# Performance work log

Measured on AMD Instinct MI355X. Metric: run time of the kernel, lower is better.

## Reference

```python
import jax, jax.numpy as jnp
import numpy as np

NUM_EXPERTS = 16
TOP_K = 2
FFT_LEN = 512
SEQ_LEN = 512
PRED_LEN = 720
MOE_TEMP = 1.0


def setup_inputs() -> dict:
    key = jax.random.key(0)
    ks = jax.random.split(key, 5)
    x = jax.random.normal(ks[0], (8192, SEQ_LEN), dtype=jnp.float32)
    # gating network: Linear(fft_len//2 -> num_experts)
    gw = jax.random.normal(ks[1], (NUM_EXPERTS, FFT_LEN // 2), dtype=jnp.float32) * (1.0 / np.sqrt(FFT_LEN // 2))
    gb = jnp.zeros((NUM_EXPERTS,), dtype=jnp.float32)
    # experts: RLinear = instance-norm (RevIN) + Linear(seq->pred), stacked
    ew = jax.random.normal(ks[2], (NUM_EXPERTS, SEQ_LEN, PRED_LEN), dtype=jnp.float32) * (1.0 / np.sqrt(SEQ_LEN))
    eb = jnp.zeros((NUM_EXPERTS, PRED_LEN), dtype=jnp.float32)
    return {"x": x, "gw": gw, "gb": gb, "ew": ew, "eb": eb}


def periodogram(x, n):
    # x: [B, L] -> normalized power spectrum [B, n//2]
    x0 = x - jnp.mean(x, axis=1, keepdims=True)
    dft = jnp.fft.fft(x0, n=n, axis=1) / jnp.sqrt(jnp.asarray(n, x.dtype))
    I = jnp.abs(dft[:, : n // 2]) ** 2
    s = jnp.sum(I, axis=1, keepdims=True)
    s = jnp.where(s == 0, 1.0, s)
    return I / s


def expert_apply(x, ew, eb):
    # RLinear: instance normalize, linear map, de-normalize
    mu = jnp.mean(x, axis=1, keepdims=True)
    sd = jnp.std(x, axis=1, keepdims=True) + 1e-5
    xn = (x - mu) / sd  # [B, L]
    # all experts densely: [B,L] x [E,L,P] -> [E,B,P]
    y = jnp.einsum('bl,elp->ebp', xn, ew) + eb[:, None, :]
    return y * sd[None] + mu[None]  # [E, B, P]


def reference(x, gw, gb, ew, eb):
    I = periodogram(x, FFT_LEN)  # [B, n//2]
    gate = (I @ gw.T + gb) / MOE_TEMP  # eval mode: divide by temp, no noise
    topk_vals, topk_idx = jax.lax.top_k(gate, TOP_K)  # [B, k]
    gates = jax.nn.softmax(topk_vals, axis=1)  # [B, k]
    expert_out = expert_apply(x, ew, eb)  # [E, B, P]
    # gather selected experts: [B, k, P]
    sel = jnp.take_along_axis(
        jnp.transpose(expert_out, (1, 0, 2)), topk_idx[:, :, None], axis=1
    )
    return jnp.sum(gates[:, :, None] * sel, axis=1)  # [B, P]
```

## Files before the change

### kernel.cpp

```cpp
#include <hip/hip_runtime.h>
#include <hip/hip_bf16.h>
#include <math.h>

#define NEXP  16
#define SEQ   512
#define PRED  720
#define NROWS 8192
#define NFREQ 256

typedef __bf16 bf16x8 __attribute__((ext_vector_type(8)));
typedef float  f32x16 __attribute__((ext_vector_type(16)));

__device__ __forceinline__ void gload_lds16(const void* g, void* l) {
    __builtin_amdgcn_global_load_lds(
        (const __attribute__((address_space(1))) unsigned int*)g,
        (__attribute__((address_space(3))) unsigned int*)l, 16, 0, 0);
}

__global__ __launch_bounds__(256) void k_transpose_ew(const float* __restrict__ ew,
                                                      __hip_bfloat16* __restrict__ ewt)
{
    __shared__ float tile[32][33];
    const int e  = blockIdx.z;
    const int p0 = blockIdx.x * 32;
    const int l0 = blockIdx.y * 32;
    const int tx = threadIdx.x & 31;
    const int ty = threadIdx.x >> 5;
    const float* src = ew + (size_t)e * SEQ * PRED;
#pragma unroll
    for (int i = 0; i < 4; ++i) {
        int l = l0 + ty + i * 8;
        int p = p0 + tx;
        tile[ty + i * 8][tx] = (p < PRED) ? src[(size_t)l * PRED + p] : 0.f;
    }
    __syncthreads();
    __hip_bfloat16* dst = ewt + (size_t)e * PRED * SEQ;
#pragma unroll
    for (int i = 0; i < 4; ++i) {
        int p = p0 + ty + i * 8;
        int l = l0 + tx;
        if (p < PRED) dst[(size_t)p * SEQ + l] = __float2bfloat16(tile[tx][ty + i * 8]);
    }
}

__global__ __launch_bounds__(256) void k_build_dft(__hip_bfloat16* __restrict__ bthi,
                                                   __hip_bfloat16* __restrict__ btlo)
{
    const int tid  = blockIdx.x * 256 + threadIdx.x;
    const int f    = tid >> 9;
    const int lidx = tid & 511;
    const int m    = (f * lidx) & 511;

    constexpr double Cj[9] = {0.9999247018391445033, 0.9996988186962042201,
                              0.9987954562051723927, 0.9951847266721968862,
                              0.9807852804032304491, 0.9238795325112867561,
                              0.7071067811865475244, 0.0, -1.0};
    constexpr double Sj[9] = {0.0122715382857199261, 0.0245412285229122880,
                              0.0490676743274180143, 0.0980171403295606020,
                              0.1950903220161282678, 0.3826834323650897717,
                              0.7071067811865475244, 1.0, 0.0};
    double cr = 1.0, ci = 0.0;
#pragma unroll
    for (int j = 0; j < 9; ++j) {
        const bool on = (m >> j) & 1;
        const double mr = on ? Cj[j] : 1.0;
        const double mi = on ? Sj[j] : 0.0;
        const double nr = cr * mr - ci * mi;
        ci = cr * mi + ci * mr;
        cr = nr;
    }

    const size_t c0 = (size_t)(2 * f) * 512 + lidx;
    const size_t c1 = (size_t)(2 * f + 1) * 512 + lidx;
    {
        __hip_bfloat16 h = __float2bfloat16((float)cr);
        float hif = __bfloat162float(h);
        bthi[c0] = h;
        btlo[c0] = __float2bfloat16((float)(cr - (double)hif));
    }
    {
        __hip_bfloat16 h = __float2bfloat16((float)ci);
        float hif = __bfloat162float(h);
        bthi[c1] = h;
        btlo[c1] = __float2bfloat16((float)(ci - (double)hif));
    }
}

__global__ __launch_bounds__(256) void k_stats(const float* __restrict__ x,
                                               __hip_bfloat16* __restrict__ xn,
                                               __hip_bfloat16* __restrict__ xnlo,
                                               float* __restrict__ meta)
{
    const int t  = threadIdx.x;
    const int wv = t >> 6, l = t & 63;
    const int b  = blockIdx.x * 4 + wv;
    const float* xr = x + (size_t)b * SEQ;

    const float4 v0 = *(const float4*)(xr + l * 8);
    const float4 v1 = *(const float4*)(xr + l * 8 + 4);
    const double d0 = v0.x, d1 = v0.y, d2 = v0.z, d3 = v0.w;
    const double d4 = v1.x, d5 = v1.y, d6 = v1.z, d7 = v1.w;

    double s1 = ((d0 + d1) + (d2 + d3)) + ((d4 + d5) + (d6 + d7));
    double s2 = ((d0 * d0 + d1 * d1) + (d2 * d2 + d3 * d3)) +
                ((d4 * d4 + d5 * d5) + (d6 * d6 + d7 * d7));
#pragma unroll
    for (int off = 1; off < 64; off <<= 1) {
        s1 += __shfl_xor(s1, off);
        s2 += __shfl_xor(s2, off);
    }
    const double mu = s1 * (1.0 / 512.0);
    double var = s2 * (1.0 / 512.0) - mu * mu;
    if (var < 0.0) var = 0.0;
    const double sd = sqrt(var) + 1e-5, inv = 1.0 / sd;

    unsigned int hw[4], lw[4];
#define CONV(j, dj)                                                         \
    {                                                                       \
        double xnd = (dj - mu) * inv;                                       \
        __hip_bfloat16 h = __float2bfloat16((float)xnd);                    \
        float hif = __bfloat162float(h);                                    \
        __hip_bfloat16 lo = __float2bfloat16((float)(xnd - (double)hif));   \
        unsigned int hb = *(unsigned short*)&h;                             \
        unsigned int lb = *(unsigned short*)&lo;                            \
        if ((j & 1) == 0) { hw[j >> 1] = hb; lw[j >> 1] = lb; }             \
        else { hw[j >> 1] |= hb << 16; lw[j >> 1] |= lb << 16; }            \
    }
    CONV(0, d0) CONV(1, d1) CONV(2, d2) CONV(3, d3)
    CONV(4, d4) CONV(5, d5) CONV(6, d6) CONV(7, d7)
#undef CONV
    *(uint4*)(xn   + (size_t)b * SEQ + l * 8) = uint4{hw[0], hw[1], hw[2], hw[3]};
    *(uint4*)(xnlo + (size_t)b * SEQ + l * 8) = uint4{lw[0], lw[1], lw[2], lw[3]};

    if (l == 0) {
        meta[b * 4 + 0] = (float)mu;
        meta[b * 4 + 3] = (float)sd;
    }
}

__global__ __launch_bounds__(256, 2) void k_dft_gemm(
    const __hip_bfloat16* __restrict__ xn, const __hip_bfloat16* __restrict__ xnlo,
    const __hip_bfloat16* __restrict__ bthi, const __hip_bfloat16* __restrict__ btlo,
    float* __restrict__ Iout)
{
    const int rt = blockIdx.y;
    const int ct = blockIdx.x;

    __shared__ __align__(16) __hip_bfloat16 As[2][128][64];
    __shared__ __align__(16) __hip_bfloat16 Bs[2][128][64];

    const int t  = threadIdx.x;
    const int wv = t >> 6, l = t & 63;
    const int srow = l >> 3, schk = l & 7;

    size_t aoff[4], boff[4];
#pragma unroll
    for (int i = 0; i < 4; ++i) {
        const int r   = wv * 32 + i * 8 + srow;
        const int swz = (r & 7) ^ ((r & 8) >> 1);
        aoff[i] = (size_t)(rt * 128 + r) * SEQ + (size_t)(schk ^ swz) * 8;
        boff[i] = (size_t)(ct * 128 + r) * SEQ + (size_t)(schk ^ swz) * 8;
    }

#define DSTAGE(buf, kk) do {                                                   \
    const int pass_ = (kk) >> 3;                                               \
    const int koff_ = ((kk) & 7) * 64;                                         \
    const __hip_bfloat16* ap_ = (pass_ == 1) ? xnlo : xn;                      \
    const __hip_bfloat16* bp_ = (pass_ == 2) ? btlo : bthi;                    \
    _Pragma("unroll")                                                          \
    for (int i_ = 0; i_ < 4; ++i_)                                             \
        gload_lds16(ap_ + aoff[i_] + koff_, &As[buf][wv * 32 + i_ * 8][0]);    \
    _Pragma("unroll")                                                          \
    for (int i_ = 0; i_ < 4; ++i_)                                             \
        gload_lds16(bp_ + boff[i_] + koff_, &Bs[buf][wv * 32 + i_ * 8][0]);    \
} while (0)

    f32x16 acc[2][2];
#pragma unroll
    for (int mi = 0; mi < 2; ++mi)
#pragma unroll
        for (int ni = 0; ni < 2; ++ni)
#pragma unroll
            for (int q = 0; q < 16; ++q) acc[mi][ni][q] = 0.f;

    const int wrow = (wv >> 1) * 64, wcol = (wv & 1) * 64;
    const int fl = l & 31, fh = l >> 5;
    const int rswz = (fl & 7) ^ ((fl & 8) >> 1);

    DSTAGE(0, 0);
    __syncthreads();
    int cur = 0;
    for (int kt = 0; kt < 24; ++kt) {
        if (kt < 23) DSTAGE(cur ^ 1, kt + 1);
#pragma unroll
        for (int ks = 0; ks < 4; ++ks) {
            const int g  = ks * 2 + fh;
            const int cc = (g ^ rswz) * 8;
            const bf16x8 a0 = *(const bf16x8*)&As[cur][wrow + fl][cc];
            const bf16x8 a1 = *(const bf16x8*)&As[cur][wrow + 32 + fl][cc];
            const bf16x8 b0 = *(const bf16x8*)&Bs[cur][wcol + fl][cc];
            const bf16x8 b1 = *(const bf16x8*)&Bs[cur][wcol + 32 + fl][cc];
            acc[0][0] = __builtin_amdgcn_mfma_f32_32x32x16_bf16(a0, b0, acc[0][0], 0, 0, 0);
            acc[0][1] = __builtin_amdgcn_mfma_f32_32x32x16_bf16(a0, b1, acc[0][1], 0, 0, 0);
            acc[1][0] = __builtin_amdgcn_mfma_f32_32x32x16_bf16(a1, b0, acc[1][0], 0, 0, 0);
            acc[1][1] = __builtin_amdgcn_mfma_f32_32x32x16_bf16(a1, b1, acc[1][1], 0, 0, 0);
        }
        __syncthreads();
        cur ^= 1;
    }
#undef DSTAGE

    const int crow_base = 4 * fh;
#pragma unroll
    for (int ni = 0; ni < 2; ++ni) {
        const int col = ct * 128 + wcol + ni * 32 + fl;
#pragma unroll
        for (int mi = 0; mi < 2; ++mi) {
#pragma unroll
            for (int q = 0; q < 16; ++q) {
                const float v = acc[mi][ni][q];
                const float w = __shfl_xor(v, 1);
                if ((fl & 1) == 0) {
                    const int rl = wrow + mi * 32 + (q & 3) + 8 * (q >> 2) + crow_base;
                    Iout[(size_t)(rt * 128 + rl) * NFREQ + (col >> 1)] = v * v + w * w;
                }
            }
        }
    }
}

__global__ __launch_bounds__(256) void k_gatefin(const float* __restrict__ Iout,
                                                 const float* __restrict__ gw,
                                                 const float* __restrict__ gb,
                                                 float* __restrict__ meta,
                                                 int* __restrict__ eidx,
                                                 int* __restrict__ redo,
                                                 int* __restrict__ nredo)
{
    __shared__ float gws[NEXP * 257];
    __shared__ float Pw[4][256];
    __shared__ float Gs[4][16];

    const int t  = threadIdx.x;
    const int wv = t >> 6, l = t & 63;
    const int b  = blockIdx.x * 4 + wv;

    for (int i = t; i < NEXP * NFREQ; i += 256)
        gws[(i >> 8) * 257 + (i & 255)] = gw[i];
    __syncthreads();

    const float* Ir = Iout + (size_t)b * NFREQ;
    const float i0 = Ir[l], i1 = Ir[64 + l], i2 = Ir[128 + l], i3 = Ir[192 + l];
    Pw[wv][l] = i0; Pw[wv][64 + l] = i1; Pw[wv][128 + l] = i2; Pw[wv][192 + l] = i3;
    float ps = (i0 + i1) + (i2 + i3);
#pragma unroll
    for (int off = 1; off < 64; off <<= 1) ps += __shfl_xor(ps, off);

    const int e = l >> 2, kb = l & 3;
    float acc = 0.f;
#pragma unroll 8
    for (int j = 0; j < 64; ++j) {
        const int k = kb + 4 * j;
        acc += Pw[wv][k] * gws[e * 257 + k];
    }
    acc += __shfl_xor(acc, 1);
    acc += __shfl_xor(acc, 2);
    if (kb == 0) Gs[wv][e] = acc;

    if (l == 0) {
        const float sdiv  = (ps == 0.f) ? 1.f : ps;
        const float inv_s = 1.f / sdiv;
        float b1 = -1e30f, b2 = -1e30f, b3 = -1e30f;
        int i1b = 0, i2b = 0;
#pragma unroll
        for (int i = 0; i < NEXP; ++i) {
            float v = Gs[wv][i] * inv_s + gb[i];
            if (v > b1)      { b3 = b2; b2 = b1; i2b = i1b; b1 = v; i1b = i; }
            else if (v > b2) { b3 = b2; b2 = v; i2b = i; }
            else if (v > b3) { b3 = v; }
        }
        if (b2 - b3 < 1e-4f * fmaxf(1.f, fabsf(b1))) {
            const int r = atomicAdd(nredo, 1);
            redo[r] = b;
        } else {
            const float sd = meta[b * 4 + 3];
            const float ee = __expf(b2 - b1);
            const float w0 = 1.f / (1.f + ee);
            const float w1 = ee / (1.f + ee);
            meta[b * 4 + 1] = w0 * sd;
            meta[b * 4 + 2] = w1 * sd;
            eidx[b * 2 + 0] = i1b;
            eidx[b * 2 + 1] = i2b;
        }
    }
}

__global__ __launch_bounds__(256, 4) void k_gate64(const float* __restrict__ x,
                                                   const float* __restrict__ gw,
                                                   const float* __restrict__ gb,
                                                   float* __restrict__ meta,
                                                   int* __restrict__ eidx,
                                                   const int* __restrict__ redo,
                                                   const int* __restrict__ nredo)
{
    __shared__ double Pw[4][256];
    __shared__ double Gs[4][16];

    const int t  = threadIdx.x;
    const int wv = t >> 6, l = t & 63;
    const int n  = *nredo;

    for (int it = blockIdx.x * 4 + wv; it < n; it += gridDim.x * 4) {
        const int b = redo[it];
        const float* xr = x + (size_t)b * SEQ;

        double s1 = 0.0, s2 = 0.0;
#define DLOADV(n_) double vr##n_ = (double)xr[64 * n_ + l]; s1 += vr##n_; s2 += vr##n_ * vr##n_;
        DLOADV(0) DLOADV(1) DLOADV(2) DLOADV(3) DLOADV(4) DLOADV(5) DLOADV(6) DLOADV(7)
#undef DLOADV
        double vi0, vi1, vi2, vi3, vi4, vi5, vi6, vi7;

#pragma unroll
        for (int off = 1; off < 64; off <<= 1) {
            s1 += __shfl_xor(s1, off);
            s2 += __shfl_xor(s2, off);
        }
        const double mu = s1 * (1.0 / 512.0);
        double var = s2 * (1.0 / 512.0) - mu * mu;
        if (var < 0.0) var = 0.0;
        const double sd = sqrt(var) + 1e-5;

#define DSUB(n_) vr##n_ -= mu;
        DSUB(0) DSUB(1) DSUB(2) DSUB(3) DSUB(4) DSUB(5) DSUB(6) DSUB(7)
#undef DSUB

        {
            const double C = 0.70710678118654752440084436210485;
            double a0 = vr0 + vr4, a1 = vr1 + vr5, a2 = vr2 + vr6, a3 = vr3 + vr7;
            double d0 = vr0 - vr4, d1 = vr1 - vr5, d2 = vr2 - vr6, d3 = vr3 - vr7;
            double c0 = a0 + a2, c2 = a0 - a2, c1 = a1 + a3;
            double c3i = a3 - a1;
            double e1r = C * (d1 - d3), e1i = -C * (d1 + d3);
            vr0 = c0 + c1;   vi0 = 0.0;
            vr1 = c0 - c1;   vi1 = 0.0;
            vr2 = c2;        vi2 = c3i;
            vr3 = c2;        vi3 = -c3i;
            vr4 = d0 + e1r;  vi4 = -d2 + e1i;
            vr5 = d0 - e1r;  vi5 = -d2 - e1i;
            vr6 = d0 - e1r;  vi6 =  d2 + e1i;
            vr7 = d0 + e1r;  vi7 =  d2 - e1i;
        }

        double w1r = 1.0, w1i = 0.0;
        {
            constexpr double Cr[6] = {0.9999247018391445033, 0.9996988186962042201,
                                      0.9987954562051723927, 0.9951847266721968862,
                                      0.9807852804032304491, 0.9238795325112867561};
            constexpr double Ci[6] = {-0.0122715382857199261, -0.0245412285229122880,
                                      -0.0490676743274180143, -0.0980171403295606020,
                                      -0.1950903220161282678, -0.3826834323650897717};
#pragma unroll
            for (int j = 0; j < 6; ++j) {
                const bool on = (l >> j) & 1;
                const double mr = on ? Cr[j] : 1.0;
                const double mi = on ? Ci[j] : 0.0;
                const double nr = w1r * mr - w1i * mi;
                w1i = w1r * mi + w1i * mr;
                w1r = nr;
            }
        }

        {
            double wkr = w1r, wki = w1i;
#define DTWID(n_) { double tr_ = vr##n_ * wkr - vi##n_ * wki; \
                    vi##n_ = vr##n_ * wki + vi##n_ * wkr; vr##n_ = tr_; }
#define DWSTEP() { double nr_ = wkr * w1r - wki * w1i; \
                   wki = wkr * w1i + wki * w1r; wkr = nr_; }
            DTWID(4) DWSTEP() DTWID(2) DWSTEP() DTWID(6) DWSTEP() DTWID(1)
            DWSTEP() DTWID(5) DWSTEP() DTWID(3) DWSTEP() DTWID(7)
#undef DTWID
#undef DWSTEP
        }

        double twr, twi;
        {
            double w2r = w1r * w1r - w1i * w1i, w2i = 2.0 * w1r * w1i;
            double w4r = w2r * w2r - w2i * w2i, w4i = 2.0 * w2r * w2i;
            twr = w4r * w4r - w4i * w4i; twi = 2.0 * w4r * w4i;
        }
#define DBF(R, I, h, hi, ter, tei) { \
        double br_ = __shfl_xor(R, h); double bi_ = __shfl_xor(I, h); \
        double dr_ = hi ? (R - br_) : (R + br_); \
        double di_ = hi ? (I - bi_) : (I + bi_); \
        R = dr_ * ter - di_ * tei; I = dr_ * tei + di_ * ter; }
#define DSTAGE(hc) { \
        const bool hi_ = (l & hc) != 0; \
        const double ter_ = hi_ ? twr : 1.0; \
        const double tei_ = hi_ ? twi : 0.0; \
        DBF(vr0, vi0, hc, hi_, ter_, tei_) DBF(vr1, vi1, hc, hi_, ter_, tei_) \
        DBF(vr2, vi2, hc, hi_, ter_, tei_) DBF(vr3, vi3, hc, hi_, ter_, tei_) \
        DBF(vr4, vi4, hc, hi_, ter_, tei_) DBF(vr5, vi5, hc, hi_, ter_, tei_) \
        DBF(vr6, vi6, hc, hi_, ter_, tei_) DBF(vr7, vi7, hc, hi_, ter_, tei_) \
        double ntr_ = twr * twr - twi * twi; twi = 2.0 * twr * twi; twr = ntr_; }
        DSTAGE(32) DSTAGE(16) DSTAGE(8) DSTAGE(4) DSTAGE(2) DSTAGE(1)
#undef DSTAGE
#undef DBF

        const int k2 = (int)(__brev((unsigned)l) >> 26);
        double ps = 0.0;
        if ((l & 1) == 0) {
            const int kb = 8 * k2;
            double P;
            P = vr0 * vr0 + vi0 * vi0; ps += P; Pw[wv][0 + kb] = P;
            P = vr1 * vr1 + vi1 * vi1; ps += P; Pw[wv][4 + kb] = P;
            P = vr2 * vr2 + vi2 * vi2; ps += P; Pw[wv][2 + kb] = P;
            P = vr3 * vr3 + vi3 * vi3; ps += P; Pw[wv][6 + kb] = P;
            P = vr4 * vr4 + vi4 * vi4; ps += P; Pw[wv][1 + kb] = P;
            P = vr5 * vr5 + vi5 * vi5; ps += P; Pw[wv][5 + kb] = P;
            P = vr6 * vr6 + vi6 * vi6; ps += P; Pw[wv][3 + kb] = P;
            P = vr7 * vr7 + vi7 * vi7; ps += P; Pw[wv][7 + kb] = P;
        }
#pragma unroll
        for (int off = 1; off < 64; off <<= 1) ps += __shfl_xor(ps, off);

        {
            const int e = l >> 2, kb = l & 3;
            double acc = 0.0;
#pragma unroll 8
            for (int j = 0; j < 64; ++j) {
                int k = kb + 4 * j;
                acc += Pw[wv][k] * (double)gw[e * NFREQ + k];
            }
            acc += __shfl_xor(acc, 1);
            acc += __shfl_xor(acc, 2);
            if (kb == 0) Gs[wv][e] = acc;
        }

        if (l == 0) {
            const double sdiv  = (ps == 0.0) ? 1.0 : ps;
            const double inv_s = 1.0 / sdiv;
            double best = -1e300, best2 = -1e300;
            int i0b = 0, i1b = 0;
#pragma unroll
            for (int i = 0; i < NEXP; ++i) {
                double v = Gs[wv][i] * inv_s + (double)gb[i];
                if (v > best)       { best2 = best; i1b = i0b; best = v; i0b = i; }
                else if (v > best2) { best2 = v; i1b = i; }
            }
            const double eexp = (double)__expf((float)(best2 - best));
            const double w0 = 1.0 / (1.0 + eexp);
            const double w1 = eexp / (1.0 + eexp);
            meta[b * 4 + 0] = (float)mu;
            meta[b * 4 + 1] = (float)(w0 * sd);
            meta[b * 4 + 2] = (float)(w1 * sd);
            meta[b * 4 + 3] = (float)sd;
            eidx[b * 2 + 0] = i0b;
            eidx[b * 2 + 1] = i1b;
        }
    }
}

__global__ __launch_bounds__(256) void k_count(const int* __restrict__ eidx,
                                               int* __restrict__ blockHist)
{
    __shared__ int h[32];
    const int t   = threadIdx.x;
    const int blk = blockIdx.x;
    if (t < 32) h[t] = 0;
    __syncthreads();
    const int b  = blk * 256 + t;
    const int e0 = eidx[2 * b];
    const int e1 = eidx[2 * b + 1];
    atomicAdd(&h[e0], 1);
    atomicAdd(&h[16 + e1], 1);
    __syncthreads();
    if (t < 32) blockHist[(t >> 4) * 512 + blk * 16 + (t & 15)] = h[t];
}

__global__ void k_scan(const int* __restrict__ blockHist, int* __restrict__ counts,
                       int* __restrict__ offs, int* __restrict__ toff,
                       int* __restrict__ base)
{
    __shared__ int cnt[32];
    __shared__ int off_s[32];
    const int j = threadIdx.x;
    if (j < 32) {
        const int s = j >> 4, e = j & 15;
        int acc = 0;
        for (int blk = 0; blk < 32; ++blk) acc += blockHist[s * 512 + blk * 16 + e];
        cnt[j] = acc;
        counts[j] = acc;
    }
    __syncthreads();
    if (j < 2) {
        int acc = 0, tac = 0;
        for (int i = 0; i < NEXP; ++i) {
            const int c = cnt[j * 16 + i];
            off_s[j * 16 + i] = acc;
            offs[j * 16 + i]  = acc;
            acc += c;
            toff[j * 17 + i] = tac;
            tac += (c + 127) >> 7;
        }
        toff[j * 17 + 16] = tac;
    }
    __syncthreads();
    if (j < 32) {
        const int s = j >> 4, e = j & 15;
        int run = off_s[j];
        for (int blk = 0; blk < 32; ++blk) {
            base[s * 512 + blk * 16 + e] = run;
            run += blockHist[s * 512 + blk * 16 + e];
        }
    }
}

__global__ __launch_bounds__(256) void k_scatter(const int* __restrict__ eidx,
                                                 const int* __restrict__ base,
                                                 int* __restrict__ lists)
{
    __shared__ int whist[2][4][16];
    const int t   = threadIdx.x;
    const int wv  = t >> 6, l = t & 63;
    const int blk = blockIdx.x;
    const int b   = blk * 256 + t;
    const int e0  = eidx[2 * b];
    const int e1  = eidx[2 * b + 1];
    const unsigned long long before = (1ULL << l) - 1ULL;

    unsigned long long m0 = 0, m1 = 0;
#pragma unroll
    for (int bb = 0; bb < 16; ++bb) {
        unsigned long long m = __ballot(e0 == bb);
        if (e0 == bb) m0 = m;
        if (l == 0) whist[0][wv][bb] = __popcll(m);
    }
#pragma unroll
    for (int bb = 0; bb < 16; ++bb) {
        unsigned long long m = __ballot(e1 == bb);
        if (e1 == bb) m1 = m;
        if (l == 0) whist[1][wv][bb] = __popcll(m);
    }
    __syncthreads();

    int p0 = __popcll(m0 & before);
    int p1 = __popcll(m1 & before);
    for (int w = 0; w < 4; ++w) {
        if (w < wv) {
            p0 += whist[0][w][e0];
            p1 += whist[1][w][e1];
        }
    }
    lists[base[blk * 16 + e0] + p0]                 = b;
    lists[NROWS + base[512 + blk * 16 + e1] + p1]   = b;
}

template <int SLOT>
__global__ __launch_bounds__(256, 2) void k_expert_gemm(
    const __hip_bfloat16* __restrict__ xn, const __hip_bfloat16* __restrict__ ewt,
    const float* __restrict__ eb, const float* __restrict__ meta,
    const int* __restrict__ lists, const int* __restrict__ offs,
    const int* __restrict__ counts, const int* __restrict__ toff,
    float* __restrict__ out)
{
    const int tid = blockIdx.y;
    if (tid >= toff[SLOT * 17 + 16]) return;
    int e = 0;
#pragma unroll
    for (int i = 0; i < 15; ++i) e += (toff[SLOT * 17 + e + 1] <= tid) ? 1 : 0;
    const int rt  = tid - toff[SLOT * 17 + e];
    const int ct  = blockIdx.x;
    const int n_e = counts[SLOT * NEXP + e];

    __shared__ __align__(16) __hip_bfloat16 As[2][128][64];
    __shared__ __align__(16) __hip_bfloat16 Bs[2][128][64];
    __shared__ int   rowB[128];
    __shared__ float rowMu[128];
    __shared__ float rowC[128];

    const int t  = threadIdx.x;
    const int wv = t >> 6, l = t & 63;
    const int* list = lists + SLOT * NROWS + offs[SLOT * NEXP + e];
    if (t < 128) {
        int r  = rt * 128 + t;
        int bb = (r < n_e) ? list[r] : -1;
        rowB[t]  = bb;
        rowMu[t] = (bb >= 0) ? meta[bb * 4] : 0.f;
        rowC[t]  = (bb >= 0) ? meta[bb * 4 + 1 + SLOT] : 0.f;
    }
    __syncthreads();

    const int srow = l >> 3;
    const int schk = l & 7;
    const __hip_bfloat16* asrc[4];
    const __hip_bfloat16* bsrc[4];
#pragma unroll
    for (int i = 0; i < 4; ++i) {
        const int r   = wv * 32 + i * 8 + srow;
        const int swz = (r & 7) ^ ((r & 8) >> 1);
        const int ab  = rowB[r];
        asrc[i] = xn + ((ab >= 0) ? (size_t)ab * SEQ : 0) + (size_t)(schk ^ swz) * 8;
        const int gc  = ct * 128 + r;
        const int gcc = (gc < PRED) ? gc : (PRED - 1);
        bsrc[i] = ewt + ((size_t)e * PRED + gcc) * SEQ + (size_t)(schk ^ swz) * 8;
    }

#define STAGE(buf, koff) do {                                              \
    _Pragma("unroll")                                                      \
    for (int i_ = 0; i_ < 4; ++i_)                                         \
        gload_lds16(asrc[i_] + (koff), &As[buf][wv * 32 + i_ * 8][0]);     \
    _Pragma("unroll")                                                      \
    for (int i_ = 0; i_ < 4; ++i_)                                         \
        gload_lds16(bsrc[i_] + (koff), &Bs[buf][wv * 32 + i_ * 8][0]);     \
} while (0)

    f32x16 acc[2][2];
#pragma unroll
    for (int mi = 0; mi < 2; ++mi)
#pragma unroll
        for (int ni = 0; ni < 2; ++ni)
#pragma unroll
            for (int q = 0; q < 16; ++q) acc[mi][ni][q] = 0.f;

    const int wrow = (wv >> 1) * 64, wcol = (wv & 1) * 64;
    const int fl = l & 31, fh = l >> 5;
    const int rswz = (fl & 7) ^ ((fl & 8) >> 1);

    STAGE(0, 0);
    __syncthreads();
    int cur = 0;
    for (int kt = 0; kt < 8; ++kt) {
        if (kt < 7) STAGE(cur ^ 1, (kt + 1) * 64);
#pragma unroll
        for (int ks = 0; ks < 4; ++ks) {
            const int g  = ks * 2 + fh;
            const int cc = (g ^ rswz) * 8;
            const bf16x8 a0 = *(const bf16x8*)&As[cur][wrow + fl][cc];
            const bf16x8 a1 = *(const bf16x8*)&As[cur][wrow + 32 + fl][cc];
            const bf16x8 b0 = *(const bf16x8*)&Bs[cur][wcol + fl][cc];
            const bf16x8 b1 = *(const bf16x8*)&Bs[cur][wcol + 32 + fl][cc];
            acc[0][0] = __builtin_amdgcn_mfma_f32_32x32x16_bf16(a0, b0, acc[0][0], 0, 0, 0);
            acc[0][1] = __builtin_amdgcn_mfma_f32_32x32x16_bf16(a0, b1, acc[0][1], 0, 0, 0);
            acc[1][0] = __builtin_amdgcn_mfma_f32_32x32x16_bf16(a1, b0, acc[1][0], 0, 0, 0);
            acc[1][1] = __builtin_amdgcn_mfma_f32_32x32x16_bf16(a1, b1, acc[1][1], 0, 0, 0);
        }
        __syncthreads();
        cur ^= 1;
    }
#undef STAGE

    const int crow_base = 4 * fh;
#pragma unroll
    for (int ni = 0; ni < 2; ++ni) {
        const int col = ct * 128 + wcol + ni * 32 + fl;
        const bool cok = (col < PRED);
        const float ebv = cok ? eb[e * PRED + col] : 0.f;
#pragma unroll
        for (int mi = 0; mi < 2; ++mi) {
#pragma unroll
            for (int q = 0; q < 16; ++q) {
                const int rl = wrow + mi * 32 + (q & 3) + 8 * (q >> 2) + crow_base;
                const int bb = rowB[rl];
                if (!cok || bb < 0) continue;
                const float v = acc[mi][ni][q] + ebv;
                float* op = out + (size_t)bb * PRED + col;
                if (SLOT == 0) *op = rowMu[rl] + rowC[rl] * v;
                else           *op += rowC[rl] * v;
            }
        }
    }
}

extern "C" void kernel_launch(void* const* d_in, const int* in_sizes, int n_in,
                              void* d_out, int out_size, void* d_ws, size_t ws_size,
                              hipStream_t stream)
{
    const float* x  = (const float*)d_in[0];
    const float* gw = (const float*)d_in[1];
    const float* gb = (const float*)d_in[2];
    const float* ew = (const float*)d_in[3];
    const float* eb = (const float*)d_in[4];
    float* out = (float*)d_out;
    char*  ws  = (char*)d_ws;

    constexpr size_t XN_OFF   = 0;
    constexpr size_t XN_SZ    = (size_t)NROWS * SEQ * 2;
    constexpr size_t XNLO_OFF = XN_OFF + XN_SZ;
    constexpr size_t EWT_OFF  = XNLO_OFF + XN_SZ;
    constexpr size_t EWT_SZ   = (size_t)NEXP * PRED * SEQ * 2;
    constexpr size_t BTHI_OFF = EWT_OFF + EWT_SZ;
    constexpr size_t BT_SZ    = (size_t)512 * 512 * 2;
    constexpr size_t BTLO_OFF = BTHI_OFF + BT_SZ;
    constexpr size_t IOUT_OFF = BTLO_OFF + BT_SZ;
    constexpr size_t IOUT_SZ  = (size_t)NROWS * NFREQ * 4;
    constexpr size_t META_OFF = IOUT_OFF + IOUT_SZ;
    constexpr size_t META_SZ  = (size_t)NROWS * 4 * 4;
    constexpr size_t EIDX_OFF = META_OFF + META_SZ;
    constexpr size_t EIDX_SZ  = (size_t)NROWS * 2 * 4;
    constexpr size_t LIST_OFF = EIDX_OFF + EIDX_SZ;
    constexpr size_t LIST_SZ  = (size_t)2 * NROWS * 4;
    constexpr size_t CNT_OFF  = LIST_OFF + LIST_SZ;
    constexpr size_t OFFS_OFF = CNT_OFF + 144;
    constexpr size_t TOFF_OFF = OFFS_OFF + 128;
    constexpr size_t BH_OFF   = TOFF_OFF + 160;
    constexpr size_t BASE_OFF = BH_OFF + 4096;
    constexpr size_t REDO_OFF = BASE_OFF + 4096;

    __hip_bfloat16* xn   = (__hip_bfloat16*)(ws + XN_OFF);
    __hip_bfloat16* xnlo = (__hip_bfloat16*)(ws + XNLO_OFF);
    __hip_bfloat16* ewt  = (__hip_bfloat16*)(ws + EWT_OFF);
    __hip_bfloat16* bthi = (__hip_bfloat16*)(ws + BTHI_OFF);
    __hip_bfloat16* btlo = (__hip_bfloat16*)(ws + BTLO_OFF);
    float* Iout  = (float*)(ws + IOUT_OFF);
    float* meta  = (float*)(ws + META_OFF);
    int* eidx    = (int*)(ws + EIDX_OFF);
    int* lists   = (int*)(ws + LIST_OFF);
    int* counts  = (int*)(ws + CNT_OFF);
    int* nredo   = (int*)(ws + CNT_OFF + 128);
    int* offs    = (int*)(ws + OFFS_OFF);
    int* toff    = (int*)(ws + TOFF_OFF);
    int* bhist   = (int*)(ws + BH_OFF);
    int* base    = (int*)(ws + BASE_OFF);
    int* redo    = (int*)(ws + REDO_OFF);

    hipMemsetAsync(counts, 0, 144, stream);

    k_build_dft<<<dim3(512), dim3(256), 0, stream>>>(bthi, btlo);
    k_transpose_ew<<<dim3(23, 16, NEXP), dim3(256), 0, stream>>>(ew, ewt);
    k_stats<<<dim3(NROWS / 4), dim3(256), 0, stream>>>(x, xn, xnlo, meta);
    k_dft_gemm<<<dim3(4, 64), dim3(256), 0, stream>>>(xn, xnlo, bthi, btlo, Iout);
    k_gatefin<<<dim3(NROWS / 4), dim3(256), 0, stream>>>(Iout, gw, gb, meta, eidx,
                                                         redo, nredo);
    k_gate64<<<dim3(64), dim3(256), 0, stream>>>(x, gw, gb, meta, eidx, redo, nredo);
    k_count<<<dim3(32), dim3(256), 0, stream>>>(eidx, bhist);
    k_scan<<<dim3(1), dim3(64), 0, stream>>>(bhist, counts, offs, toff, base);
    k_scatter<<<dim3(32), dim3(256), 0, stream>>>(eidx, base, lists);
    k_expert_gemm<0><<<dim3(6, 80), dim3(256), 0, stream>>>(
        xn, ewt, eb, meta, lists, offs, counts, toff, out);
    k_expert_gemm<1><<<dim3(6, 80), dim3(256), 0, stream>>>(
        xn, ewt, eb, meta, lists, offs, counts, toff, out);
}
```

Before: 166.7 us.

## Halve GEMM row tiles to 64 and raise occupancy for DFT and expert GEMMs

Shrinks the M tile of both the DFT GEMM and the routed expert GEMM from 128 to 64 rows. Each wave now computes a 32x64 sub-tile, and launch bounds go from 2 to 3 blocks per CU. The grids double to match, and the per-expert tile count in the scan now uses 64-row tiles, which cuts padding waste for unevenly loaded experts. It also drops a memset by having the DFT-building kernel zero the redo counter. The cost is less reuse of each B tile per block, so B-operand global and LDS traffic rises.

```diff
diff --git a/kernel.cpp b/kernel.cpp
--- a/kernel.cpp
+++ b/kernel.cpp
@@ -44,8 +44,11 @@
 }
 
 __global__ __launch_bounds__(256) void k_build_dft(__hip_bfloat16* __restrict__ bthi,
-                                                   __hip_bfloat16* __restrict__ btlo)
-{
+                                                   __hip_bfloat16* __restrict__ btlo,
+                                                   int* __restrict__ nredo)
+{
+    if (blockIdx.x == 0 && threadIdx.x == 0) *nredo = 0;
+
     const int tid  = blockIdx.x * 256 + threadIdx.x;
     const int f    = tid >> 9;
     const int lidx = tid & 511;
@@ -138,7 +141,7 @@
     }
 }
 
-__global__ __launch_bounds__(256, 2) void k_dft_gemm(
+__global__ __launch_bounds__(256, 3) void k_dft_gemm(
     const __hip_bfloat16* __restrict__ xn, const __hip_bfloat16* __restrict__ xnlo,
     const __hip_bfloat16* __restrict__ bthi, const __hip_bfloat16* __restrict__ btlo,
     float* __restrict__ Iout)
@@ -146,20 +149,25 @@
     const int rt = blockIdx.y;
     const int ct = blockIdx.x;
 
-    __shared__ __align__(16) __hip_bfloat16 As[2][128][64];
+    __shared__ __align__(16) __hip_bfloat16 As[2][64][64];
     __shared__ __align__(16) __hip_bfloat16 Bs[2][128][64];
 
     const int t  = threadIdx.x;
     const int wv = t >> 6, l = t & 63;
-    const int srow = l >> 3, schk = l & 7;
-
-    size_t aoff[4], boff[4];
+    const int trow = t >> 3, tchk = t & 7;
+
+    size_t aoff[2], boff[4];
+#pragma unroll
+    for (int i = 0; i < 2; ++i) {
+        const int r   = i * 32 + trow;
+        const int swz = (r & 7) ^ ((r & 8) >> 1);
+        aoff[i] = (size_t)(rt * 64 + r) * SEQ + (size_t)(tchk ^ swz) * 8;
+    }
 #pragma unroll
     for (int i = 0; i < 4; ++i) {
-        const int r   = wv * 32 + i * 8 + srow;
+        const int r   = i * 32 + trow;
         const int swz = (r & 7) ^ ((r & 8) >> 1);
-        aoff[i] = (size_t)(rt * 128 + r) * SEQ + (size_t)(schk ^ swz) * 8;
-        boff[i] = (size_t)(ct * 128 + r) * SEQ + (size_t)(schk ^ swz) * 8;
+        boff[i] = (size_t)(ct * 128 + r) * SEQ + (size_t)(tchk ^ swz) * 8;
     }
 
 #define DSTAGE(buf, kk) do {                                                   \
@@ -168,22 +176,20 @@
     const __hip_bfloat16* ap_ = (pass_ == 1) ? xnlo : xn;                      \
     const __hip_bfloat16* bp_ = (pass_ == 2) ? btlo : bthi;                    \
     _Pragma("unroll")                                                          \
-    for (int i_ = 0; i_ < 4; ++i_)                                             \
-        gload_lds16(ap_ + aoff[i_] + koff_, &As[buf][wv * 32 + i_ * 8][0]);    \
+    for (int i_ = 0; i_ < 2; ++i_)                                             \
+        gload_lds16(ap_ + aoff[i_] + koff_, &As[buf][i_ * 32 + wv * 8][0]);    \
     _Pragma("unroll")                                                          \
     for (int i_ = 0; i_ < 4; ++i_)                                             \
-        gload_lds16(bp_ + boff[i_] + koff_, &Bs[buf][wv * 32 + i_ * 8][0]);    \
+        gload_lds16(bp_ + boff[i_] + koff_, &Bs[buf][i_ * 32 + wv * 8][0]);    \
 } while (0)
 
-    f32x16 acc[2][2];
-#pragma unroll
-    for (int mi = 0; mi < 2; ++mi)
-#pragma unroll
-        for (int ni = 0; ni < 2; ++ni)
-#pragma unroll
-            for (int q = 0; q < 16; ++q) acc[mi][ni][q] = 0.f;
-
-    const int wrow = (wv >> 1) * 64, wcol = (wv & 1) * 64;
+    f32x16 acc[2];
+#pragma unroll
+    for (int ni = 0; ni < 2; ++ni)
+#pragma unroll
+        for (int q = 0; q < 16; ++q) acc[ni][q] = 0.f;
+
+    const int wr = wv >> 1, wc = wv & 1;
     const int fl = l & 31, fh = l >> 5;
     const int rswz = (fl & 7) ^ ((fl & 8) >> 1);
 
@@ -196,14 +202,11 @@
         for (int ks = 0; ks < 4; ++ks) {
             const int g  = ks * 2 + fh;
             const int cc = (g ^ rswz) * 8;
-            const bf16x8 a0 = *(const bf16x8*)&As[cur][wrow + fl][cc];
-            const bf16x8 a1 = *(const bf16x8*)&As[cur][wrow + 32 + fl][cc];
-            const bf16x8 b0 = *(const bf16x8*)&Bs[cur][wcol + fl][cc];
-            const bf16x8 b1 = *(const bf16x8*)&Bs[cur][wcol + 32 + fl][cc];
-            acc[0][0] = __builtin_amdgcn_mfma_f32_32x32x16_bf16(a0, b0, acc[0][0], 0, 0, 0);
-            acc[0][1] = __builtin_amdgcn_mfma_f32_32x32x16_bf16(a0, b1, acc[0][1], 0, 0, 0);
-            acc[1][0] = __builtin_amdgcn_mfma_f32_32x32x16_bf16(a1, b0, acc[1][0], 0, 0, 0);
-            acc[1][1] = __builtin_amdgcn_mfma_f32_32x32x16_bf16(a1, b1, acc[1][1], 0, 0, 0);
+            const bf16x8 a  = *(const bf16x8*)&As[cur][wr * 32 + fl][cc];
+            const bf16x8 b0 = *(const bf16x8*)&Bs[cur][wc * 64 + fl][cc];
+            const bf16x8 b1 = *(const bf16x8*)&Bs[cur][wc * 64 + 32 + fl][cc];
+            acc[0] = __builtin_amdgcn_mfma_f32_32x32x16_bf16(a, b0, acc[0], 0, 0, 0);
+            acc[1] = __builtin_amdgcn_mfma_f32_32x32x16_bf16(a, b1, acc[1], 0, 0, 0);
         }
         __syncthreads();
         cur ^= 1;
@@ -213,17 +216,14 @@
     const int crow_base = 4 * fh;
 #pragma unroll
     for (int ni = 0; ni < 2; ++ni) {
-        const int col = ct * 128 + wcol + ni * 32 + fl;
-#pragma unroll
-        for (int mi = 0; mi < 2; ++mi) {
-#pragma unroll
-            for (int q = 0; q < 16; ++q) {
-                const float v = acc[mi][ni][q];
-                const float w = __shfl_xor(v, 1);
-                if ((fl & 1) == 0) {
-                    const int rl = wrow + mi * 32 + (q & 3) + 8 * (q >> 2) + crow_base;
-                    Iout[(size_t)(rt * 128 + rl) * NFREQ + (col >> 1)] = v * v + w * w;
-                }
+        const int col = ct * 128 + wc * 64 + ni * 32 + fl;
+#pragma unroll
+        for (int q = 0; q < 16; ++q) {
+            const float v = acc[ni][q];
+            const float w = __shfl_xor(v, 1);
+            if ((fl & 1) == 0) {
+                const int rl = wr * 32 + (q & 3) + 8 * (q >> 2) + crow_base;
+                Iout[(size_t)(rt * 64 + rl) * NFREQ + (col >> 1)] = v * v + w * w;
             }
         }
     }
@@ -500,7 +500,7 @@
             offs[j * 16 + i]  = acc;
             acc += c;
             toff[j * 17 + i] = tac;
-            tac += (c + 127) >> 7;
+            tac += (c + 63) >> 6;
         }
         toff[j * 17 + 16] = tac;
     }
@@ -556,7 +556,7 @@
 }
 
 template <int SLOT>
-__global__ __launch_bounds__(256, 2) void k_expert_gemm(
+__global__ __launch_bounds__(256, 3) void k_expert_gemm(
     const __hip_bfloat16* __restrict__ xn, const __hip_bfloat16* __restrict__ ewt,
     const float* __restrict__ eb, const float* __restrict__ meta,
     const int* __restrict__ lists, const int* __restrict__ offs,
@@ -572,17 +572,17 @@
     const int ct  = blockIdx.x;
     const int n_e = counts[SLOT * NEXP + e];
 
-    __shared__ __align__(16) __hip_bfloat16 As[2][128][64];
+    __shared__ __align__(16) __hip_bfloat16 As[2][64][64];
     __shared__ __align__(16) __hip_bfloat16 Bs[2][128][64];
-    __shared__ int   rowB[128];
-    __shared__ float rowMu[128];
-    __shared__ float rowC[128];
+    __shared__ int   rowB[64];
+    __shared__ float rowMu[64];
+    __shared__ float rowC[64];
 
     const int t  = threadIdx.x;
     const int wv = t >> 6, l = t & 63;
     const int* list = lists + SLOT * NROWS + offs[SLOT * NEXP + e];
-    if (t < 128) {
-        int r  = rt * 128 + t;
+    if (t < 64) {
+        int r  = rt * 64 + t;
         int bb = (r < n_e) ? list[r] : -1;
         rowB[t]  = bb;
         rowMu[t] = (bb >= 0) ? meta[bb * 4] : 0.f;
@@ -590,39 +590,41 @@
     }
     __syncthreads();
 
-    const int srow = l >> 3;
-    const int schk = l & 7;
-    const __hip_bfloat16* asrc[4];
+    const int trow = t >> 3, tchk = t & 7;
+    const __hip_bfloat16* asrc[2];
     const __hip_bfloat16* bsrc[4];
 #pragma unroll
-    for (int i = 0; i < 4; ++i) {
-        const int r   = wv * 32 + i * 8 + srow;
+    for (int i = 0; i < 2; ++i) {
+        const int r   = i * 32 + trow;
         const int swz = (r & 7) ^ ((r & 8) >> 1);
         const int ab  = rowB[r];
-        asrc[i] = xn + ((ab >= 0) ? (size_t)ab * SEQ : 0) + (size_t)(schk ^ swz) * 8;
+        asrc[i] = xn + ((ab >= 0) ? (size_t)ab * SEQ : 0) + (size_t)(tchk ^ swz) * 8;
+    }
+#pragma unroll
+    for (int i = 0; i < 4; ++i) {
+        const int r   = i * 32 + trow;
+        const int swz = (r & 7) ^ ((r & 8) >> 1);
         const int gc  = ct * 128 + r;
         const int gcc = (gc < PRED) ? gc : (PRED - 1);
-        bsrc[i] = ewt + ((size_t)e * PRED + gcc) * SEQ + (size_t)(schk ^ swz) * 8;
+        bsrc[i] = ewt + ((size_t)e * PRED + gcc) * SEQ + (size_t)(tchk ^ swz) * 8;
     }
 
 #define STAGE(buf, koff) do {                                              \
     _Pragma("unroll")                                                      \
-    for (int i_ = 0; i_ < 4; ++i_)                                         \
-        gload_lds16(asrc[i_] + (koff), &As[buf][wv * 32 + i_ * 8][0]);     \
+    for (int i_ = 0; i_ < 2; ++i_)                                         \
+        gload_lds16(asrc[i_] + (koff), &As[buf][i_ * 32 + wv * 8][0]);     \
     _Pragma("unroll")                                                      \
     for (int i_ = 0; i_ < 4; ++i_)                                         \
-        gload_lds16(bsrc[i_] + (koff), &Bs[buf][wv * 32 + i_ * 8][0]);     \
+        gload_lds16(bsrc[i_] + (koff), &Bs[buf][i_ * 32 + wv * 8][0]);     \
 } while (0)
 
-    f32x16 acc[2][2];
-#pragma unroll
-    for (int mi = 0; mi < 2; ++mi)
-#pragma unroll
-        for (int ni = 0; ni < 2; ++ni)
-#pragma unroll
-            for (int q = 0; q < 16; ++q) acc[mi][ni][q] = 0.f;
-
-    const int wrow = (wv >> 1) * 64, wcol = (wv & 1) * 64;
+    f32x16 acc[2];
+#pragma unroll
+    for (int ni = 0; ni < 2; ++ni)
+#pragma unroll
+        for (int q = 0; q < 16; ++q) acc[ni][q] = 0.f;
+
+    const int wr = wv >> 1, wc = wv & 1;
     const int fl = l & 31, fh = l >> 5;
     const int rswz = (fl & 7) ^ ((fl & 8) >> 1);
 
@@ -635,14 +637,11 @@
         for (int ks = 0; ks < 4; ++ks) {
             const int g  = ks * 2 + fh;
             const int cc = (g ^ rswz) * 8;
-            const bf16x8 a0 = *(const bf16x8*)&As[cur][wrow + fl][cc];
-            const bf16x8 a1 = *(const bf16x8*)&As[cur][wrow + 32 + fl][cc];
-            const bf16x8 b0 = *(const bf16x8*)&Bs[cur][wcol + fl][cc];
-            const bf16x8 b1 = *(const bf16x8*)&Bs[cur][wcol + 32 + fl][cc];
-            acc[0][0] = __builtin_amdgcn_mfma_f32_32x32x16_bf16(a0, b0, acc[0][0], 0, 0, 0);
-            acc[0][1] = __builtin_amdgcn_mfma_f32_32x32x16_bf16(a0, b1, acc[0][1], 0, 0, 0);
-            acc[1][0] = __builtin_amdgcn_mfma_f32_32x32x16_bf16(a1, b0, acc[1][0], 0, 0, 0);
-            acc[1][1] = __builtin_amdgcn_mfma_f32_32x32x16_bf16(a1, b1, acc[1][1], 0, 0, 0);
+            const bf16x8 a  = *(const bf16x8*)&As[cur][wr * 32 + fl][cc];
+            const bf16x8 b0 = *(const bf16x8*)&Bs[cur][wc * 64 + fl][cc];
+            const bf16x8 b1 = *(const bf16x8*)&Bs[cur][wc * 64 + 32 + fl][cc];
+            acc[0] = __builtin_amdgcn_mfma_f32_32x32x16_bf16(a, b0, acc[0], 0, 0, 0);
+            acc[1] = __builtin_amdgcn_mfma_f32_32x32x16_bf16(a, b1, acc[1], 0, 0, 0);
         }
         __syncthreads();
         cur ^= 1;
@@ -652,21 +651,18 @@
     const int crow_base = 4 * fh;
 #pragma unroll
     for (int ni = 0; ni < 2; ++ni) {
-        const int col = ct * 128 + wcol + ni * 32 + fl;
+        const int col = ct * 128 + wc * 64 + ni * 32 + fl;
         const bool cok = (col < PRED);
         const float ebv = cok ? eb[e * PRED + col] : 0.f;
 #pragma unroll
-        for (int mi = 0; mi < 2; ++mi) {
-#pragma unroll
-            for (int q = 0; q < 16; ++q) {
-                const int rl = wrow + mi * 32 + (q & 3) + 8 * (q >> 2) + crow_base;
-                const int bb = rowB[rl];
-                if (!cok || bb < 0) continue;
-                const float v = acc[mi][ni][q] + ebv;
-                float* op = out + (size_t)bb * PRED + col;
-                if (SLOT == 0) *op = rowMu[rl] + rowC[rl] * v;
-                else           *op += rowC[rl] * v;
-            }
+        for (int q = 0; q < 16; ++q) {
+            const int rl = wr * 32 + (q & 3) + 8 * (q >> 2) + crow_base;
+            const int bb = rowB[rl];
+            if (!cok || bb < 0) continue;
+            const float v = acc[ni][q] + ebv;
+            float* op = out + (size_t)bb * PRED + col;
+            if (SLOT == 0) *op = rowMu[rl] + rowC[rl] * v;
+            else           *op += rowC[rl] * v;
         }
     }
 }
@@ -723,20 +719,18 @@
     int* base    = (int*)(ws + BASE_OFF);
     int* redo    = (int*)(ws + REDO_OFF);
 
-    hipMemsetAsync(counts, 0, 144, stream);
-
-    k_build_dft<<<dim3(512), dim3(256), 0, stream>>>(bthi, btlo);
+    k_build_dft<<<dim3(512), dim3(256), 0, stream>>>(bthi, btlo, nredo);
     k_transpose_ew<<<dim3(23, 16, NEXP), dim3(256), 0, stream>>>(ew, ewt);
     k_stats<<<dim3(NROWS / 4), dim3(256), 0, stream>>>(x, xn, xnlo, meta);
-    k_dft_gemm<<<dim3(4, 64), dim3(256), 0, stream>>>(xn, xnlo, bthi, btlo, Iout);
+    k_dft_gemm<<<dim3(4, 128), dim3(256), 0, stream>>>(xn, xnlo, bthi, btlo, Iout);
     k_gatefin<<<dim3(NROWS / 4), dim3(256), 0, stream>>>(Iout, gw, gb, meta, eidx,
                                                          redo, nredo);
     k_gate64<<<dim3(64), dim3(256), 0, stream>>>(x, gw, gb, meta, eidx, redo, nredo);
     k_count<<<dim3(32), dim3(256), 0, stream>>>(eidx, bhist);
     k_scan<<<dim3(1), dim3(64), 0, stream>>>(bhist, counts, offs, toff, base);
     k_scatter<<<dim3(32), dim3(256), 0, stream>>>(eidx, base, lists);
-    k_expert_gemm<0><<<dim3(6, 80), dim3(256), 0, stream>>>(
+    k_expert_gemm<0><<<dim3(6, 160), dim3(256), 0, stream>>>(
         xn, ewt, eb, meta, lists, offs, counts, toff, out);
-    k_expert_gemm<1><<<dim3(6, 80), dim3(256), 0, stream>>>(
+    k_expert_gemm<1><<<dim3(6, 160), dim3(256), 0, stream>>>(
         xn, ewt, eb, meta, lists, offs, counts, toff, out);
 }
```

After: 178.1 us. 6.8% more time.
